# Kernel optimization log

Hardware: AMD Instinct MI355X
Metric: run time of the kernel (lower is better)

The kernel has to match this reference:

```python
import jax, jax.numpy as jnp
import numpy as np

B, S, D_VAL, D_AT = 4, 4096, 256, 256


def setup_inputs() -> dict:
    key = jax.random.key(0)
    k1, k2, k3, k4 = jax.random.split(key, 4)
    x = jax.random.normal(k1, (B, S, D_VAL), dtype=jnp.float32)
    # nn.Linear(d_in, d_out, bias=False) weight has shape [d_out, d_in]; y = x @ W.T
    Wq = jax.random.normal(k2, (D_AT, D_VAL), dtype=jnp.float32) * (1.0 / np.sqrt(D_VAL))
    Wk = jax.random.normal(k3, (D_AT, D_VAL), dtype=jnp.float32) * (1.0 / np.sqrt(D_VAL))
    Wv = jax.random.normal(k4, (D_VAL, D_VAL), dtype=jnp.float32) * (1.0 / np.sqrt(D_VAL))
    return {"x": x, "Wq": Wq, "Wk": Wk, "Wv": Wv}


def reference(x, Wq, Wk, Wv):
    # projections (Linear, no bias): x @ W.T
    q = jnp.einsum('bsd,ad->bsa', x, Wq)   # [B,S,d_at]
    k = jnp.einsum('bsd,ad->bsa', x, Wk)   # [B,S,d_at]
    v = jnp.einsum('bsd,ed->bse', x, Wv)   # [B,S,d_val]
    scale = 1.0 / jnp.sqrt(jnp.asarray(q.shape[-1], dtype=q.dtype))
    scores = jnp.einsum('bqa,bka->bqk', q, k) * scale  # [B,S,S]
    weights = jax.nn.softmax(scores, axis=-1)
    out = jnp.einsum('bqk,bke->bqe', weights, v)       # [B,S,d_val]
    return out
```

## Files before the change

kernel.cpp:

```cpp
#include <hip/hip_runtime.h>
#include <stdint.h>

#define B_ 4
#define S_ 4096
#define D_ 256
#define M_ (B_*S_)

typedef __attribute__((ext_vector_type(8))) short bf16x8;
typedef __attribute__((ext_vector_type(4))) float f32x4;
typedef __attribute__((ext_vector_type(4))) unsigned short u16x4;

static __device__ __forceinline__ unsigned short f2bf(float f) {
  union { float f; unsigned u; } v; v.f = f;
  unsigned r = v.u + 0x7fffu + ((v.u >> 16) & 1u);
  return (unsigned short)(r >> 16);
}

__global__ void cvt_kernel(const float* __restrict__ src, unsigned short* __restrict__ dst,
                           int n4) {
  int i = blockIdx.x * blockDim.x + threadIdx.x;
  int stride = gridDim.x * blockDim.x;
  for (; i < n4; i += stride) {
    float4 v = reinterpret_cast<const float4*>(src)[i];
    u16x4 o;
    o.x = f2bf(v.x); o.y = f2bf(v.y);
    o.z = f2bf(v.z); o.w = f2bf(v.w);
    reinterpret_cast<u16x4*>(dst)[i] = o;
  }
}

__global__ void cvt_w_kernel(const float* __restrict__ Wq, const float* __restrict__ Wk,
                             const float* __restrict__ Wv,
                             unsigned short* __restrict__ wqb, unsigned short* __restrict__ wkb,
                             unsigned short* __restrict__ wvb) {
  const int m = blockIdx.y;
  const float* src = (m == 0) ? Wq : (m == 1) ? Wk : Wv;
  unsigned short* dst = (m == 0) ? wqb : (m == 1) ? wkb : wvb;
  const float scale = (m == 0) ? 0.0625f * 1.44269504f : 1.0f;
  int i = blockIdx.x * 256 + threadIdx.x;
  float4 v = reinterpret_cast<const float4*>(src)[i];
  u16x4 o;
  o.x = f2bf(v.x * scale); o.y = f2bf(v.y * scale);
  o.z = f2bf(v.z * scale); o.w = f2bf(v.w * scale);
  reinterpret_cast<u16x4*>(dst)[i] = o;
}

__global__ __launch_bounds__(256) void proj_kernel(
    const unsigned short* __restrict__ xb,
    const unsigned short* __restrict__ wq,
    const unsigned short* __restrict__ wk,
    const unsigned short* __restrict__ wv,
    unsigned short* __restrict__ q_ws,
    unsigned short* __restrict__ k_ws,
    unsigned short* __restrict__ vt_ws) {
  __shared__ char lw[65536];
  const int mat = blockIdx.y;
  const unsigned short* wb = (mat == 0) ? wq : (mat == 1) ? wk : wv;
  const int bx = blockIdx.x;
  const int rt = bx >> 1, ch = bx & 1;
  const int tid = threadIdx.x;
  const int wave = tid >> 6, lane = tid & 63;
  const int lr = lane & 15, lh = lane >> 4;
  const int row0 = rt * 64 + wave * 16;

  {
    const char* wg = reinterpret_cast<const char*>(wb) + ch * 65536;
    #pragma unroll
    for (int i = 0; i < 16; i++) {
      int off = i * 4096 + tid * 16;
      int r = off >> 9, c = off & 511;
      int src = r * 512 + (c ^ ((r & 7) << 4));
      __builtin_amdgcn_global_load_lds(
        (__attribute__((address_space(1))) void*)(void*)(wg + src),
        (__attribute__((address_space(3))) void*)(lw + off),
        16, 0, 0);
    }
  }
  __syncthreads();

  const f32x4 zero = {0.f, 0.f, 0.f, 0.f};

  bf16x8 af[8];
  {
    const unsigned short* xp = xb + (size_t)(row0 + lr) * D_ + lh * 8;
    #pragma unroll
    for (int kc = 0; kc < 8; kc++)
      af[kc] = *reinterpret_cast<const bf16x8*>(xp + kc * 32);
  }

  f32x4 acc[8];
  #pragma unroll
  for (int n = 0; n < 8; n++) acc[n] = zero;

  #pragma unroll
  for (int kc = 0; kc < 8; kc++) {
    #pragma unroll
    for (int n = 0; n < 8; n++) {
      int wrow = n * 16 + lr;
      bf16x8 bfv = *reinterpret_cast<const bf16x8*>(
          lw + wrow * 512 + ((kc * 64 + lh * 16) ^ ((wrow & 7) << 4)));
      acc[n] = __builtin_amdgcn_mfma_f32_16x16x32_bf16(af[kc], bfv, acc[n], 0, 0, 0);
    }
  }

  const int b  = row0 >> 12;
  const int s0 = row0 & 4095;
  const int t2 = s0 >> 5;
  const int w1 = wave & 1;

  if (mat == 0) {
    #pragma unroll
    for (int n = 0; n < 8; n++) {
      int col = ch * 128 + n * 16 + lr;
      #pragma unroll
      for (int r = 0; r < 4; r++) {
        int row = row0 + lh * 4 + r;
        q_ws[(size_t)row * D_ + col] = f2bf(acc[n][r]);
      }
    }
  } else if (mat == 1) {
    char* tb = reinterpret_cast<char*>(k_ws) + ((size_t)(b * 128 + t2)) * 16384;
    #pragma unroll
    for (int n = 0; n < 8; n++) {
      int ng = ch * 8 + n;
      int base = (w1 * 8 + (ng >> 1)) * 1024 +
                 (((ng & 1) << 1) | (lr >> 3)) * 256 +
                 lh * 64 + (lr & 7) * 2;
      #pragma unroll
      for (int r = 0; r < 4; r++)
        *reinterpret_cast<unsigned short*>(tb + base + r * 16) = f2bf(acc[n][r]);
    }
  } else {
    char* tb = reinterpret_cast<char*>(vt_ws) + ((size_t)(b * 128 + t2)) * 16384;
    #pragma unroll
    for (int n = 0; n < 8; n++) {
      int ng = ch * 8 + n;
      u16x4 o;
      o.x = f2bf(acc[n][0]); o.y = f2bf(acc[n][1]);
      o.z = f2bf(acc[n][2]); o.w = f2bf(acc[n][3]);
      *reinterpret_cast<u16x4*>(tb + ng * 1024 + lh * 256 + lr * 16 + w1 * 8) = o;
    }
  }
}

__global__ __launch_bounds__(256, 2) void attn_kernel(
    const unsigned short* __restrict__ q_ws,
    const unsigned short* __restrict__ k_ws,
    const unsigned short* __restrict__ vt_ws,
    float* __restrict__ po, float* __restrict__ pm, float* __restrict__ pl) {
  __shared__ char lds[2][32768];

  const int bid0 = blockIdx.x;
  const int xcd = bid0 & 7, qt = bid0 >> 3;
  const int b = xcd >> 1, h = xcd & 1;
  const int tid = threadIdx.x;
  const int wave = tid >> 6, lane = tid & 63;
  const int lr = lane & 15, lh = lane >> 4;

  const int qrow0 = b * S_ + qt * 128 + wave * 32;

  bf16x8 qfA[8], qfB[8];
  {
    const unsigned short* qpA = q_ws + (size_t)(qrow0 + lr) * D_ + lh * 8;
    const unsigned short* qpB = qpA + 16 * D_;
    #pragma unroll
    for (int kc = 0; kc < 8; kc++) {
      qfA[kc] = *reinterpret_cast<const bf16x8*>(qpA + kc * 32);
      qfB[kc] = *reinterpret_cast<const bf16x8*>(qpB + kc * 32);
    }
  }

  f32x4 oaccA[16], oaccB[16];
  const f32x4 zero = {0.f, 0.f, 0.f, 0.f};
  #pragma unroll
  for (int n = 0; n < 16; n++) { oaccA[n] = zero; oaccB[n] = zero; }
  float mA = -1e30f, mB = -1e30f, lA = 0.f, lB = 0.f;

  const char* kgb = reinterpret_cast<const char*>(k_ws) + ((size_t)(b * 128 + h * 64)) * 16384;
  const char* vgb = reinterpret_cast<const char*>(vt_ws) + ((size_t)(b * 128 + h * 64)) * 16384;

  auto stage = [&](int t, int buf) {
    const char* kg = kgb + (size_t)t * 16384;
    const char* vg = vgb + (size_t)t * 16384;
    char* lk = lds[buf];
    char* lv = lds[buf] + 16384;
    #pragma unroll
    for (int i = 0; i < 4; i++) {
      __builtin_amdgcn_global_load_lds(
        (__attribute__((address_space(1))) void*)(void*)(kg + i * 4096 + tid * 16),
        (__attribute__((address_space(3))) void*)(lk + i * 4096 + tid * 16),
        16, 0, 0);
    }
    #pragma unroll
    for (int i = 0; i < 4; i++) {
      __builtin_amdgcn_global_load_lds(
        (__attribute__((address_space(1))) void*)(void*)(vg + i * 4096 + tid * 16),
        (__attribute__((address_space(3))) void*)(lv + i * 4096 + tid * 16),
        16, 0, 0);
    }
  };

  stage(0, 0);
  __syncthreads();

  for (int t = 0; t < 64; t++) {
    const int cur = t & 1;
    if (t + 1 < 64) stage(t + 1, cur ^ 1);

    const char* lk = lds[cur];
    const char* lv = lds[cur] + 16384;

    f32x4 sA0 = zero, sA1 = zero, sB0 = zero, sB1 = zero;
    #pragma unroll
    for (int kc = 0; kc < 8; kc++) {
      bf16x8 kf0 = *reinterpret_cast<const bf16x8*>(lk + kc * 1024 + lane * 16);
      bf16x8 kf1 = *reinterpret_cast<const bf16x8*>(lk + (8 + kc) * 1024 + lane * 16);
      sA0 = __builtin_amdgcn_mfma_f32_16x16x32_bf16(kf0, qfA[kc], sA0, 0, 0, 0);
      sA1 = __builtin_amdgcn_mfma_f32_16x16x32_bf16(kf1, qfA[kc], sA1, 0, 0, 0);
      sB0 = __builtin_amdgcn_mfma_f32_16x16x32_bf16(kf0, qfB[kc], sB0, 0, 0, 0);
      sB1 = __builtin_amdgcn_mfma_f32_16x16x32_bf16(kf1, qfB[kc], sB1, 0, 0, 0);
    }

    float pmaxA = fmaxf(fmaxf(fmaxf(sA0[0], sA0[1]), fmaxf(sA0[2], sA0[3])),
                        fmaxf(fmaxf(sA1[0], sA1[1]), fmaxf(sA1[2], sA1[3])));
    float pmaxB = fmaxf(fmaxf(fmaxf(sB0[0], sB0[1]), fmaxf(sB0[2], sB0[3])),
                        fmaxf(fmaxf(sB1[0], sB1[1]), fmaxf(sB1[2], sB1[3])));
    pmaxA = fmaxf(pmaxA, __shfl_xor(pmaxA, 16));
    pmaxA = fmaxf(pmaxA, __shfl_xor(pmaxA, 32));
    pmaxB = fmaxf(pmaxB, __shfl_xor(pmaxB, 16));
    pmaxB = fmaxf(pmaxB, __shfl_xor(pmaxB, 32));

    if (!__all((pmaxA - mA <= 8.f) & (pmaxB - mB <= 8.f))) {
      float miA = fmaxf(mA, pmaxA), miB = fmaxf(mB, pmaxB);
      float aA = exp2f(mA - miA), aB = exp2f(mB - miB);
      mA = miA; mB = miB; lA *= aA; lB *= aB;
      #pragma unroll
      for (int r = 0; r < 4; r++) {
        float avA = __shfl(aA, lh * 4 + r);
        float avB = __shfl(aB, lh * 4 + r);
        #pragma unroll
        for (int n = 0; n < 16; n++) { oaccA[n][r] *= avA; oaccB[n][r] *= avB; }
      }
    }

    bf16x8 paA, paB;
    float sumA = 0.f, sumB = 0.f;
    #pragma unroll
    for (int j = 0; j < 8; j++) {
      float vA = (j < 4) ? sA0[j & 3] : sA1[j & 3];
      float vB = (j < 4) ? sB0[j & 3] : sB1[j & 3];
      float pA = exp2f(vA - mA);
      float pB = exp2f(vB - mB);
      sumA += pA; sumB += pB;
      paA[j] = (short)f2bf(pA);
      paB[j] = (short)f2bf(pB);
    }
    sumA += __shfl_xor(sumA, 16); sumA += __shfl_xor(sumA, 32);
    sumB += __shfl_xor(sumB, 16); sumB += __shfl_xor(sumB, 32);
    lA += sumA; lB += sumB;

    #pragma unroll
    for (int n = 0; n < 16; n++) {
      bf16x8 vf = *reinterpret_cast<const bf16x8*>(lv + n * 1024 + lane * 16);
      oaccA[n] = __builtin_amdgcn_mfma_f32_16x16x32_bf16(paA, vf, oaccA[n], 0, 0, 0);
      oaccB[n] = __builtin_amdgcn_mfma_f32_16x16x32_bf16(paB, vf, oaccB[n], 0, 0, 0);
    }

    __syncthreads();
  }

  const size_t hoff = (size_t)h * 16384;
  #pragma unroll
  for (int n = 0; n < 16; n++) {
    int col = n * 16 + lr;
    #pragma unroll
    for (int r = 0; r < 4; r++) {
      po[(hoff + qrow0 + lh * 4 + r) * D_ + col] = oaccA[n][r];
      po[(hoff + qrow0 + 16 + lh * 4 + r) * D_ + col] = oaccB[n][r];
    }
  }
  if (lh == 0) { pm[hoff + qrow0 + lr] = mA; pl[hoff + qrow0 + lr] = lA; }
  if (lh == 1) { pm[hoff + qrow0 + 16 + lr] = mB; pl[hoff + qrow0 + 16 + lr] = lB; }
}

__global__ __launch_bounds__(256) void merge_kernel(
    const float* __restrict__ po, const float* __restrict__ pm,
    const float* __restrict__ pl, float* __restrict__ out) {
  int idx = blockIdx.x * 256 + threadIdx.x;
  int row = idx >> 6, c4 = idx & 63;
  float m0 = pm[row], m1 = pm[16384 + row];
  float l0 = pl[row], l1 = pl[16384 + row];
  float M = fmaxf(m0, m1);
  float a0 = exp2f(m0 - M), a1 = exp2f(m1 - M);
  float inv = 1.0f / (l0 * a0 + l1 * a1);
  float4 o0 = reinterpret_cast<const float4*>(po)[(size_t)row * 64 + c4];
  float4 o1 = reinterpret_cast<const float4*>(po)[(size_t)(16384 + row) * 64 + c4];
  float4 o;
  o.x = (o0.x * a0 + o1.x * a1) * inv;
  o.y = (o0.y * a0 + o1.y * a1) * inv;
  o.z = (o0.z * a0 + o1.z * a1) * inv;
  o.w = (o0.w * a0 + o1.w * a1) * inv;
  reinterpret_cast<float4*>(out)[(size_t)row * 64 + c4] = o;
}

extern "C" void kernel_launch(void* const* d_in, const int* in_sizes, int n_in,
                              void* d_out, int out_size, void* d_ws, size_t ws_size,
                              hipStream_t stream) {
  const float* x  = (const float*)d_in[0];
  const float* Wq = (const float*)d_in[1];
  const float* Wk = (const float*)d_in[2];
  const float* Wv = (const float*)d_in[3];
  float* out = (float*)d_out;

  char* ws = (char*)d_ws;
  unsigned short* xb    = (unsigned short*)(ws);
  unsigned short* wqb   = (unsigned short*)(ws + 8388608);
  unsigned short* wkb   = (unsigned short*)(ws + 8519680);
  unsigned short* wvb   = (unsigned short*)(ws + 8650752);
  unsigned short* q_ws  = (unsigned short*)(ws + 8781824);
  unsigned short* k_ws  = (unsigned short*)(ws + 17170432);
  unsigned short* vt_ws = (unsigned short*)(ws + 25559040);
  float*          po    = (float*)(ws + 33947648);
  float*          pm    = (float*)(ws + 67502080);
  float*          pl    = (float*)(ws + 67633152);

  cvt_kernel<<<1024, 256, 0, stream>>>(x, xb, M_ * D_ / 4);
  cvt_w_kernel<<<dim3(64, 3), 256, 0, stream>>>(Wq, Wk, Wv, wqb, wkb, wvb);
  proj_kernel<<<dim3(512, 3), 256, 0, stream>>>(xb, wqb, wkb, wvb, q_ws, k_ws, vt_ws);
  attn_kernel<<<256, 256, 0, stream>>>(q_ws, k_ws, vt_ws, po, pm, pl);
  merge_kernel<<<4096, 256, 0, stream>>>(po, pm, pl, out);
}
```

Baseline: 206.1 us.

## Split attention KV into four chunks, bf16 partials, fragment-packed projection weights

The attention kernel now splits the key range into four chunks instead of two and launches 512 blocks, so more CUs are busy. Partial outputs are staged through LDS and written as coalesced bf16 rather than fp32, and the merge kernel combines four partials. The projection kernel drops its LDS weight staging and reads weights that cvt_w_kernel pre-packs in MFMA fragment order, with each block computing all 256 output columns. The MFMA sections also get s_setprio hints. This adds bf16 rounding of the partial outputs and more merge traffic, in exchange for parallelism and less write bandwidth.

New measurement: 183.0 us. -11.2%, faster.

```diff
diff --git a/kernel.cpp b/kernel.cpp
--- a/kernel.cpp
+++ b/kernel.cpp
@@ -7,6 +7,7 @@
 #define M_ (B_*S_)
 
 typedef __attribute__((ext_vector_type(8))) short bf16x8;
+typedef __attribute__((ext_vector_type(8))) unsigned short u16x8;
 typedef __attribute__((ext_vector_type(4))) float f32x4;
 typedef __attribute__((ext_vector_type(4))) unsigned short u16x4;
 
@@ -14,6 +15,10 @@
   union { float f; unsigned u; } v; v.f = f;
   unsigned r = v.u + 0x7fffu + ((v.u >> 16) & 1u);
   return (unsigned short)(r >> 16);
+}
+static __device__ __forceinline__ float bf2f(unsigned short h) {
+  union { unsigned u; float f; } v; v.u = ((unsigned)h) << 16;
+  return v.f;
 }
 
 __global__ void cvt_kernel(const float* __restrict__ src, unsigned short* __restrict__ dst,
@@ -38,14 +43,21 @@
   unsigned short* dst = (m == 0) ? wqb : (m == 1) ? wkb : wvb;
   const float scale = (m == 0) ? 0.0625f * 1.44269504f : 1.0f;
   int i = blockIdx.x * 256 + threadIdx.x;
-  float4 v = reinterpret_cast<const float4*>(src)[i];
-  u16x4 o;
-  o.x = f2bf(v.x * scale); o.y = f2bf(v.y * scale);
-  o.z = f2bf(v.z * scale); o.w = f2bf(v.w * scale);
-  reinterpret_cast<u16x4*>(dst)[i] = o;
-}
-
-__global__ __launch_bounds__(256) void proj_kernel(
+  int frag = i >> 6, lane = i & 63;
+  int kc = frag >> 4, n = frag & 15;
+  int lr = lane & 15, lh = lane >> 4;
+  const float* sp = src + (size_t)(n * 16 + lr) * D_ + kc * 32 + lh * 8;
+  float4 a = reinterpret_cast<const float4*>(sp)[0];
+  float4 b = reinterpret_cast<const float4*>(sp)[1];
+  u16x8 o;
+  o[0] = f2bf(a.x * scale); o[1] = f2bf(a.y * scale);
+  o[2] = f2bf(a.z * scale); o[3] = f2bf(a.w * scale);
+  o[4] = f2bf(b.x * scale); o[5] = f2bf(b.y * scale);
+  o[6] = f2bf(b.z * scale); o[7] = f2bf(b.w * scale);
+  *reinterpret_cast<u16x8*>(dst + (size_t)frag * 512 + lane * 8) = o;
+}
+
+__global__ __launch_bounds__(256, 3) void proj_kernel(
     const unsigned short* __restrict__ xb,
     const unsigned short* __restrict__ wq,
     const unsigned short* __restrict__ wk,
@@ -53,30 +65,12 @@
     unsigned short* __restrict__ q_ws,
     unsigned short* __restrict__ k_ws,
     unsigned short* __restrict__ vt_ws) {
-  __shared__ char lw[65536];
   const int mat = blockIdx.y;
   const unsigned short* wb = (mat == 0) ? wq : (mat == 1) ? wk : wv;
-  const int bx = blockIdx.x;
-  const int rt = bx >> 1, ch = bx & 1;
   const int tid = threadIdx.x;
   const int wave = tid >> 6, lane = tid & 63;
   const int lr = lane & 15, lh = lane >> 4;
-  const int row0 = rt * 64 + wave * 16;
-
-  {
-    const char* wg = reinterpret_cast<const char*>(wb) + ch * 65536;
-    #pragma unroll
-    for (int i = 0; i < 16; i++) {
-      int off = i * 4096 + tid * 16;
-      int r = off >> 9, c = off & 511;
-      int src = r * 512 + (c ^ ((r & 7) << 4));
-      __builtin_amdgcn_global_load_lds(
-        (__attribute__((address_space(1))) void*)(void*)(wg + src),
-        (__attribute__((address_space(3))) void*)(lw + off),
-        16, 0, 0);
-    }
-  }
-  __syncthreads();
+  const int row0 = blockIdx.x * 64 + wave * 16;
 
   const f32x4 zero = {0.f, 0.f, 0.f, 0.f};
 
@@ -88,18 +82,16 @@
       af[kc] = *reinterpret_cast<const bf16x8*>(xp + kc * 32);
   }
 
-  f32x4 acc[8];
-  #pragma unroll
-  for (int n = 0; n < 8; n++) acc[n] = zero;
+  f32x4 acc[16];
+  #pragma unroll
+  for (int n = 0; n < 16; n++) acc[n] = zero;
 
   #pragma unroll
   for (int kc = 0; kc < 8; kc++) {
     #pragma unroll
-    for (int n = 0; n < 8; n++) {
-      int wrow = n * 16 + lr;
-      bf16x8 bfv = *reinterpret_cast<const bf16x8*>(
-          lw + wrow * 512 + ((kc * 64 + lh * 16) ^ ((wrow & 7) << 4)));
-      acc[n] = __builtin_amdgcn_mfma_f32_16x16x32_bf16(af[kc], bfv, acc[n], 0, 0, 0);
+    for (int n = 0; n < 16; n++) {
+      bf16x8 wf = *reinterpret_cast<const bf16x8*>(wb + (size_t)(kc * 16 + n) * 512 + lane * 8);
+      acc[n] = __builtin_amdgcn_mfma_f32_16x16x32_bf16(af[kc], wf, acc[n], 0, 0, 0);
     }
   }
 
@@ -110,8 +102,8 @@
 
   if (mat == 0) {
     #pragma unroll
-    for (int n = 0; n < 8; n++) {
-      int col = ch * 128 + n * 16 + lr;
+    for (int n = 0; n < 16; n++) {
+      int col = n * 16 + lr;
       #pragma unroll
       for (int r = 0; r < 4; r++) {
         int row = row0 + lh * 4 + r;
@@ -121,10 +113,9 @@
   } else if (mat == 1) {
     char* tb = reinterpret_cast<char*>(k_ws) + ((size_t)(b * 128 + t2)) * 16384;
     #pragma unroll
-    for (int n = 0; n < 8; n++) {
-      int ng = ch * 8 + n;
-      int base = (w1 * 8 + (ng >> 1)) * 1024 +
-                 (((ng & 1) << 1) | (lr >> 3)) * 256 +
+    for (int n = 0; n < 16; n++) {
+      int base = (w1 * 8 + (n >> 1)) * 1024 +
+                 (((n & 1) << 1) | (lr >> 3)) * 256 +
                  lh * 64 + (lr & 7) * 2;
       #pragma unroll
       for (int r = 0; r < 4; r++)
@@ -133,12 +124,11 @@
   } else {
     char* tb = reinterpret_cast<char*>(vt_ws) + ((size_t)(b * 128 + t2)) * 16384;
     #pragma unroll
-    for (int n = 0; n < 8; n++) {
-      int ng = ch * 8 + n;
+    for (int n = 0; n < 16; n++) {
       u16x4 o;
       o.x = f2bf(acc[n][0]); o.y = f2bf(acc[n][1]);
       o.z = f2bf(acc[n][2]); o.w = f2bf(acc[n][3]);
-      *reinterpret_cast<u16x4*>(tb + ng * 1024 + lh * 256 + lr * 16 + w1 * 8) = o;
+      *reinterpret_cast<u16x4*>(tb + n * 1024 + lh * 256 + lr * 16 + w1 * 8) = o;
     }
   }
 }
@@ -147,12 +137,14 @@
     const unsigned short* __restrict__ q_ws,
     const unsigned short* __restrict__ k_ws,
     const unsigned short* __restrict__ vt_ws,
-    float* __restrict__ po, float* __restrict__ pm, float* __restrict__ pl) {
+    unsigned short* __restrict__ po, float* __restrict__ pm, float* __restrict__ pl) {
   __shared__ char lds[2][32768];
 
   const int bid0 = blockIdx.x;
-  const int xcd = bid0 & 7, qt = bid0 >> 3;
-  const int b = xcd >> 1, h = xcd & 1;
+  const int xcd = bid0 & 7, idx = bid0 >> 3;
+  const int b = xcd >> 1;
+  const int h = (xcd & 1) * 2 + (idx >> 5);
+  const int qt = idx & 31;
   const int tid = threadIdx.x;
   const int wave = tid >> 6, lane = tid & 63;
   const int lr = lane & 15, lh = lane >> 4;
@@ -176,8 +168,8 @@
   for (int n = 0; n < 16; n++) { oaccA[n] = zero; oaccB[n] = zero; }
   float mA = -1e30f, mB = -1e30f, lA = 0.f, lB = 0.f;
 
-  const char* kgb = reinterpret_cast<const char*>(k_ws) + ((size_t)(b * 128 + h * 64)) * 16384;
-  const char* vgb = reinterpret_cast<const char*>(vt_ws) + ((size_t)(b * 128 + h * 64)) * 16384;
+  const char* kgb = reinterpret_cast<const char*>(k_ws) + ((size_t)(b * 128 + h * 32)) * 16384;
+  const char* vgb = reinterpret_cast<const char*>(vt_ws) + ((size_t)(b * 128 + h * 32)) * 16384;
 
   auto stage = [&](int t, int buf) {
     const char* kg = kgb + (size_t)t * 16384;
@@ -203,14 +195,15 @@
   stage(0, 0);
   __syncthreads();
 
-  for (int t = 0; t < 64; t++) {
+  for (int t = 0; t < 32; t++) {
     const int cur = t & 1;
-    if (t + 1 < 64) stage(t + 1, cur ^ 1);
+    if (t + 1 < 32) stage(t + 1, cur ^ 1);
 
     const char* lk = lds[cur];
     const char* lv = lds[cur] + 16384;
 
     f32x4 sA0 = zero, sA1 = zero, sB0 = zero, sB1 = zero;
+    __builtin_amdgcn_s_setprio(1);
     #pragma unroll
     for (int kc = 0; kc < 8; kc++) {
       bf16x8 kf0 = *reinterpret_cast<const bf16x8*>(lk + kc * 1024 + lane * 16);
@@ -220,6 +213,7 @@
       sB0 = __builtin_amdgcn_mfma_f32_16x16x32_bf16(kf0, qfB[kc], sB0, 0, 0, 0);
       sB1 = __builtin_amdgcn_mfma_f32_16x16x32_bf16(kf1, qfB[kc], sB1, 0, 0, 0);
     }
+    __builtin_amdgcn_s_setprio(0);
 
     float pmaxA = fmaxf(fmaxf(fmaxf(sA0[0], sA0[1]), fmaxf(sA0[2], sA0[3])),
                         fmaxf(fmaxf(sA1[0], sA1[1]), fmaxf(sA1[2], sA1[3])));
@@ -259,48 +253,68 @@
     sumB += __shfl_xor(sumB, 16); sumB += __shfl_xor(sumB, 32);
     lA += sumA; lB += sumB;
 
+    __builtin_amdgcn_s_setprio(1);
     #pragma unroll
     for (int n = 0; n < 16; n++) {
       bf16x8 vf = *reinterpret_cast<const bf16x8*>(lv + n * 1024 + lane * 16);
       oaccA[n] = __builtin_amdgcn_mfma_f32_16x16x32_bf16(paA, vf, oaccA[n], 0, 0, 0);
       oaccB[n] = __builtin_amdgcn_mfma_f32_16x16x32_bf16(paB, vf, oaccB[n], 0, 0, 0);
     }
+    __builtin_amdgcn_s_setprio(0);
 
     __syncthreads();
   }
 
-  const size_t hoff = (size_t)h * 16384;
+  char* pwv = &lds[0][0] + wave * 16384;
   #pragma unroll
   for (int n = 0; n < 16; n++) {
-    int col = n * 16 + lr;
+    int colb = (n * 16 + lr) * 2;
     #pragma unroll
     for (int r = 0; r < 4; r++) {
-      po[(hoff + qrow0 + lh * 4 + r) * D_ + col] = oaccA[n][r];
-      po[(hoff + qrow0 + 16 + lh * 4 + r) * D_ + col] = oaccB[n][r];
-    }
-  }
-  if (lh == 0) { pm[hoff + qrow0 + lr] = mA; pl[hoff + qrow0 + lr] = lA; }
-  if (lh == 1) { pm[hoff + qrow0 + 16 + lr] = mB; pl[hoff + qrow0 + 16 + lr] = lB; }
+      *reinterpret_cast<unsigned short*>(pwv + (lh * 4 + r) * 512 + colb) = f2bf(oaccA[n][r]);
+      *reinterpret_cast<unsigned short*>(pwv + (16 + lh * 4 + r) * 512 + colb) = f2bf(oaccB[n][r]);
+    }
+  }
+  __syncthreads();
+  {
+    unsigned short* pob = po + ((size_t)h * 16384 + qrow0) * D_;
+    #pragma unroll
+    for (int i = 0; i < 16; i++) {
+      int off = i * 1024 + lane * 16;
+      bf16x8 v = *reinterpret_cast<const bf16x8*>(pwv + off);
+      int row = off >> 9, colb = off & 511;
+      *reinterpret_cast<bf16x8*>(reinterpret_cast<char*>(pob) + row * 512 + colb) = v;
+    }
+  }
+  if (lh == 0) { pm[(size_t)h * 16384 + qrow0 + lr] = mA; pl[(size_t)h * 16384 + qrow0 + lr] = lA; }
+  if (lh == 1) { pm[(size_t)h * 16384 + qrow0 + 16 + lr] = mB; pl[(size_t)h * 16384 + qrow0 + 16 + lr] = lB; }
 }
 
 __global__ __launch_bounds__(256) void merge_kernel(
-    const float* __restrict__ po, const float* __restrict__ pm,
+    const unsigned short* __restrict__ po, const float* __restrict__ pm,
     const float* __restrict__ pl, float* __restrict__ out) {
   int idx = blockIdx.x * 256 + threadIdx.x;
-  int row = idx >> 6, c4 = idx & 63;
-  float m0 = pm[row], m1 = pm[16384 + row];
-  float l0 = pl[row], l1 = pl[16384 + row];
-  float M = fmaxf(m0, m1);
-  float a0 = exp2f(m0 - M), a1 = exp2f(m1 - M);
-  float inv = 1.0f / (l0 * a0 + l1 * a1);
-  float4 o0 = reinterpret_cast<const float4*>(po)[(size_t)row * 64 + c4];
-  float4 o1 = reinterpret_cast<const float4*>(po)[(size_t)(16384 + row) * 64 + c4];
-  float4 o;
-  o.x = (o0.x * a0 + o1.x * a1) * inv;
-  o.y = (o0.y * a0 + o1.y * a1) * inv;
-  o.z = (o0.z * a0 + o1.z * a1) * inv;
-  o.w = (o0.w * a0 + o1.w * a1) * inv;
-  reinterpret_cast<float4*>(out)[(size_t)row * 64 + c4] = o;
+  int row = idx >> 5, c8 = idx & 31;
+  float m0 = pm[row], m1 = pm[16384 + row], m2 = pm[32768 + row], m3 = pm[49152 + row];
+  float l0 = pl[row], l1 = pl[16384 + row], l2 = pl[32768 + row], l3 = pl[49152 + row];
+  float M = fmaxf(fmaxf(m0, m1), fmaxf(m2, m3));
+  float a0 = exp2f(m0 - M), a1 = exp2f(m1 - M), a2 = exp2f(m2 - M), a3 = exp2f(m3 - M);
+  float inv = 1.0f / (l0 * a0 + l1 * a1 + l2 * a2 + l3 * a3);
+  float acc[8];
+  #pragma unroll
+  for (int j = 0; j < 8; j++) acc[j] = 0.f;
+  const float aw[4] = {a0, a1, a2, a3};
+  #pragma unroll
+  for (int hh = 0; hh < 4; hh++) {
+    u16x8 v = *reinterpret_cast<const u16x8*>(po + ((size_t)hh * 16384 + row) * D_ + c8 * 8);
+    #pragma unroll
+    for (int j = 0; j < 8; j++) acc[j] += aw[hh] * bf2f(v[j]);
+  }
+  float4 o0, o1;
+  o0.x = acc[0] * inv; o0.y = acc[1] * inv; o0.z = acc[2] * inv; o0.w = acc[3] * inv;
+  o1.x = acc[4] * inv; o1.y = acc[5] * inv; o1.z = acc[6] * inv; o1.w = acc[7] * inv;
+  float4* op = reinterpret_cast<float4*>(out + (size_t)row * D_ + c8 * 8);
+  op[0] = o0; op[1] = o1;
 }
 
 extern "C" void kernel_launch(void* const* d_in, const int* in_sizes, int n_in,
@@ -320,13 +334,13 @@
   unsigned short* q_ws  = (unsigned short*)(ws + 8781824);
   unsigned short* k_ws  = (unsigned short*)(ws + 17170432);
   unsigned short* vt_ws = (unsigned short*)(ws + 25559040);
-  float*          po    = (float*)(ws + 33947648);
+  unsigned short* po    = (unsigned short*)(ws + 33947648);
   float*          pm    = (float*)(ws + 67502080);
-  float*          pl    = (float*)(ws + 67633152);
+  float*          pl    = (float*)(ws + 67764224);
 
   cvt_kernel<<<1024, 256, 0, stream>>>(x, xb, M_ * D_ / 4);
-  cvt_w_kernel<<<dim3(64, 3), 256, 0, stream>>>(Wq, Wk, Wv, wqb, wkb, wvb);
-  proj_kernel<<<dim3(512, 3), 256, 0, stream>>>(xb, wqb, wkb, wvb, q_ws, k_ws, vt_ws);
-  attn_kernel<<<256, 256, 0, stream>>>(q_ws, k_ws, vt_ws, po, pm, pl);
-  merge_kernel<<<4096, 256, 0, stream>>>(po, pm, pl, out);
-}
+  cvt_w_kernel<<<dim3(32, 3), 256, 0, stream>>>(Wq, Wk, Wv, wqb, wkb, wvb);
+  proj_kernel<<<dim3(256, 3), 256, 0, stream>>>(xb, wqb, wkb, wvb, q_ws, k_ws, vt_ws);
+  attn_kernel<<<512, 256, 0, stream>>>(q_ws, k_ws, vt_ws, po, pm, pl);
+  merge_kernel<<<2048, 256, 0, stream>>>(po, pm, pl, out);
+}
```
